# Kernel tuning notes

Hardware: AMD Instinct MI355X
Metric: run time of the kernel (lower is better)

The kernel has to match this reference:

```python
import jax, jax.numpy as jnp
import numpy as np


def _dwconv(x, w, pad):
    # depthwise conv, x: [B,C,H,W], w: [C,1,kh,kw]
    return jax.lax.conv_general_dilated(
        x, w, (1, 1), [(pad, pad), (pad, pad)],
        dimension_numbers=('NCHW', 'OIHW', 'NCHW'),
        feature_group_count=x.shape[1])


def _hw_to_wh(x, h, w):
    # rearrange 'b (h w) c -> b (w h) c'
    b, t, c = x.shape
    return x.reshape(b, h, w, c).transpose(0, 2, 1, 3).reshape(b, t, c)


def _wkv(decay, first, k, v):
    # Vision-RWKV WKV: decay/first [C4]; k, v [B, T, C4]
    w_neg = -jnp.exp(decay)  # RUN_CUDA applies w = -exp(w)
    u = first

    def step(carry, kv):
        p, q, o = carry
        kt, vt = kv
        no = jnp.maximum(o, u + kt)
        A = jnp.exp(o - no)
        Bx = jnp.exp(u + kt - no)
        y = (A * p + Bx * vt) / (A * q + Bx)
        no2 = jnp.maximum(o + w_neg, kt)
        A2 = jnp.exp(o + w_neg - no2)
        B2 = jnp.exp(kt - no2)
        return (A2 * p + B2 * vt, A2 * q + B2, no2), y

    Bn, T, C4 = k.shape
    init = (jnp.zeros((Bn, C4), k.dtype), jnp.zeros((Bn, C4), k.dtype),
            jnp.full((Bn, C4), -1e38, k.dtype))
    _, ys = jax.lax.scan(step, init, (jnp.swapaxes(k, 0, 1), jnp.swapaxes(v, 0, 1)))
    return jnp.swapaxes(ys, 0, 1)  # [B, T, C4]


def setup_inputs() -> dict:
    key = jax.random.key(0)
    ks = jax.random.split(key, 16)
    B, H, W, C = 8, 64, 64, 256
    T = H * W
    C4 = 4 * C
    s = 1.0 / np.sqrt(C)
    return {
        'x': jax.random.normal(ks[0], (B, T, C), jnp.float32),
        'alpha': jax.random.normal(ks[1], (4,), jnp.float32) * 0.5,
        'dw1': jax.random.normal(ks[2], (C, 1, 1, 1), jnp.float32) * s,
        'dw3': jax.random.normal(ks[3], (C, 1, 3, 3), jnp.float32) * s,
        'dw5': jax.random.normal(ks[4], (C, 1, 5, 5), jnp.float32) * s,
        'Wk': jax.random.normal(ks[5], (C, C), jnp.float32) * s,
        'Wv': jax.random.normal(ks[6], (C, C), jnp.float32) * s,
        'Wr': jax.random.normal(ks[7], (C, C), jnp.float32) * s,
        'Wf': jax.random.normal(ks[8], (C, C), jnp.float32) * s,
        'bf': jax.random.normal(ks[9], (C,), jnp.float32) * 0.02,
        'Wb': jax.random.normal(ks[10], (C, C), jnp.float32) * s,
        'bb': jax.random.normal(ks[11], (C,), jnp.float32) * 0.02,
        'spatial_decay': jax.random.normal(ks[12], (C4,), jnp.float32),
        'spatial_first': jax.random.normal(ks[13], (C4,), jnp.float32),
        'Wo': jax.random.normal(ks[14], (C, C4), jnp.float32) * (1.0 / np.sqrt(C4)),
        'h': H,
        'w': W,
    }


def reference(x, alpha, dw1, dw3, dw5, Wk, Wv, Wr, Wf, bf, Wb, bb,
              spatial_decay, spatial_first, Wo, h, w):
    B, T, C = x.shape
    # OmniShift (training path): alpha-weighted identity + depthwise 1/3/5 convs
    xi = x.reshape(B, h, w, C).transpose(0, 3, 1, 2)  # [B,C,H,W]
    xsft = (alpha[0] * xi + alpha[1] * _dwconv(xi, dw1, 0)
            + alpha[2] * _dwconv(xi, dw3, 1) + alpha[3] * _dwconv(xi, dw5, 2))
    xf = xsft.transpose(0, 2, 3, 1).reshape(B, T, C)  # [B,T,C]
    k = xf @ Wk.T
    v = xf @ Wv.T
    sr = jax.nn.sigmoid(xf @ Wr.T)
    # 1x1 conv1d over channels == linear with bias
    k1 = k @ Wf.T + bf
    v1 = v @ Wf.T + bf
    k3 = k @ Wb.T + bb
    v3 = v @ Wb.T + bb
    k2 = _hw_to_wh(k1, h, w)
    v2 = _hw_to_wh(v1, h, w)
    k4 = _hw_to_wh(k3, h, w)
    v4 = _hw_to_wh(v3, h, w)
    ks_ = jnp.concatenate([k1, k2, k3, k4], axis=2)  # [B,T,4C]
    vs_ = jnp.concatenate([v1, v2, v3, v4], axis=2)
    srs = jnp.concatenate([sr, sr, sr, sr], axis=2)
    Tf = jnp.asarray(T, x.dtype)
    xs = _wkv(spatial_decay / Tf, spatial_first / Tf, ks_, vs_)
    return (xs * srs) @ Wo.T  # [B,T,C]
```

## Files before the change

kernel.cpp:

```cpp
#include <hip/hip_runtime.h>

typedef __attribute__((ext_vector_type(8))) short bf16x8;
typedef __attribute__((ext_vector_type(4))) float f32x4;
typedef __attribute__((ext_vector_type(4))) unsigned short u16x4;
typedef __attribute__((ext_vector_type(2))) unsigned short u16x2;
typedef __attribute__((ext_vector_type(8))) unsigned short u16x8;

#define GLD16(g, l) __builtin_amdgcn_global_load_lds( \
    (const __attribute__((address_space(1))) void*)(g), \
    (__attribute__((address_space(3))) void*)(l), 16, 0, 0)

__device__ __forceinline__ unsigned short f2bf(float f) {
  unsigned u = __float_as_uint(f);
  unsigned r = u + 0x7FFFu + ((u >> 16) & 1u);
  return (unsigned short)(r >> 16);
}
__device__ __forceinline__ float bf2f(unsigned short h) {
  return __uint_as_float(((unsigned)h) << 16);
}

template <int N>
__device__ __forceinline__ void wait_vm() {
  if constexpr (N == 0) asm volatile("s_waitcnt vmcnt(0)" ::: "memory");
  else if constexpr (N == 6) asm volatile("s_waitcnt vmcnt(6)" ::: "memory");
  else if constexpr (N == 8) asm volatile("s_waitcnt vmcnt(8)" ::: "memory");
  else static_assert(N == 0, "unsupported vmcnt");
}


__global__ void k_weff(const float* __restrict__ alpha,
                       const float* __restrict__ dw1,
                       const float* __restrict__ dw3,
                       const float* __restrict__ dw5,
                       float* __restrict__ weff) {
  int tap = blockIdx.x;
  int c = threadIdx.x;
  int dy = tap / 5, dx = tap % 5;
  float v = alpha[3] * dw5[c * 25 + tap];
  if (dy >= 1 && dy <= 3 && dx >= 1 && dx <= 3)
    v += alpha[2] * dw3[c * 9 + (dy - 1) * 3 + (dx - 1)];
  if (tap == 12) v += alpha[1] * dw1[c] + alpha[0];
  weff[tap * 256 + c] = v;
}

__global__ void k_combine(const float* __restrict__ Wk,
                          const float* __restrict__ Wv,
                          const float* __restrict__ Wr,
                          const float* __restrict__ Wf,
                          const float* __restrict__ Wb,
                          const float* __restrict__ bfv,
                          const float* __restrict__ bbv,
                          short* __restrict__ wcat,
                          float* __restrict__ bias) {
  int mat = blockIdx.x >> 8;
  int i = blockIdx.x & 255;
  int j = threadIdx.x;
  if (mat == 4) {
    wcat[(size_t)(1024 + i) * 256 + j] = (short)f2bf(Wr[i * 256 + j]);
    if (j == 0) bias[1024 + i] = 0.f;
    return;
  }
  const float* Am = (mat & 1) ? Wb : Wf;
  const float* Bm = (mat < 2) ? Wk : Wv;
  const float* arow = Am + i * 256;
  float acc = 0.f;
  for (int m = 0; m < 256; ++m) acc += arow[m] * Bm[m * 256 + j];
  int newrow = ((mat & 1) << 9) + (i << 1) + (mat >> 1);
  wcat[(size_t)newrow * 256 + j] = (short)f2bf(acc);
  if (j == 0) bias[newrow] = (mat & 1) ? bbv[i] : bfv[i];
}

__global__ void k_wo(const float* __restrict__ Wo, short* __restrict__ wob) {
  int i = blockIdx.x * 256 + threadIdx.x;
  wob[i] = (short)f2bf(Wo[i]);
}

__global__ __launch_bounds__(256, 8)
void k_shift(const float* __restrict__ x, const float* __restrict__ weff,
             unsigned short* __restrict__ xf) {
  int c = threadIdx.x;
  int w0 = blockIdx.x * 8;
  int h0 = blockIdx.y * 2;
  int b = blockIdx.z;

  float wg[5][5];
#pragma unroll
  for (int dy = 0; dy < 5; ++dy)
#pragma unroll
    for (int dx = 0; dx < 5; ++dx)
      wg[dy][dx] = weff[(dy * 5 + dx) * 256 + c];

  const float* xb = x + (size_t)b * 4096 * 256 + c;
  int rowoff[6];
  bool rv[6];
#pragma unroll
  for (int r = 0; r < 6; ++r) {
    int y = h0 + r - 2;
    rv[r] = (y >= 0 && y < 64);
    int yc = y < 0 ? 0 : (y > 63 ? 63 : y);
    rowoff[r] = yc * 64 * 256;
  }

  float win[6][8];
#pragma unroll
  for (int j = -2; j <= 1; ++j) {
    int xx = w0 + j;
    int slot = j & 7;
    bool xv = (xx >= 0);
    int xc = xx < 0 ? 0 : xx;
#pragma unroll
    for (int r = 0; r < 6; ++r) {
      float v = xb[rowoff[r] + xc * 256];
      win[r][slot] = (xv && rv[r]) ? v : 0.f;
    }
  }

  unsigned short* xo = xf + ((size_t)b * 4096 + (size_t)h0 * 64) * 256 + c;
#pragma unroll
  for (int ui = 0; ui < 8; ++ui) {
    int w = w0 + ui;
    {
      int xx = w + 2;
      int slot = (ui + 2) & 7;
      bool xv = (xx < 64);
      int xc = xx > 63 ? 63 : xx;
#pragma unroll
      for (int r = 0; r < 6; ++r) {
        float v = xb[rowoff[r] + xc * 256];
        win[r][slot] = (xv && rv[r]) ? v : 0.f;
      }
    }
#pragma unroll
    for (int j = 0; j < 2; ++j) {
      float a0 = 0.f, a1 = 0.f, a2 = 0.f, a3 = 0.f, a4 = 0.f;
#pragma unroll
      for (int dx = 0; dx < 5; ++dx) {
        int slot = (ui - 2 + dx) & 7;
        a0 = fmaf(win[j + 0][slot], wg[0][dx], a0);
        a1 = fmaf(win[j + 1][slot], wg[1][dx], a1);
        a2 = fmaf(win[j + 2][slot], wg[2][dx], a2);
        a3 = fmaf(win[j + 3][slot], wg[3][dx], a3);
        a4 = fmaf(win[j + 4][slot], wg[4][dx], a4);
      }
      xo[((size_t)j * 64 + w) * 256] = f2bf(((a0 + a1) + (a2 + a3)) + a4);
    }
  }
}

template <int EPI, int BM, int BK, int SWZ>
__global__ __launch_bounds__(256, (BM == 128) ? 2 : 3)
void gemm_db(const short* __restrict__ A, const short* __restrict__ Bm,
             const float* __restrict__ bias,
             void* __restrict__ O0, void* __restrict__ O1,
             int M, int N, int K) {
  constexpr int AE = BM * BK;
  constexpr int BUFS = (BM + 128) * BK;
  constexpr int MI = BM / 32;
  constexpr int CH = BK / 8;
  constexpr int LA = BM * BK / 2048;
  constexpr int LB = BK / 16;
  constexpr int LD = LA + LB;
  constexpr int RW = 132;
  __shared__ __align__(16) short lds[2 * BUFS];

  int t = threadIdx.x;
  int lane = t & 63, wv = t >> 6;
  int wr = wv >> 1, wc = wv & 1;
  int m0, n0;
  if (SWZ) {
    int x = blockIdx.x & 7;
    int j = blockIdx.x >> 3;
    m0 = (x * 32 + j / 10) * BM;
    n0 = (j % 10) * 128;
  } else {
    m0 = blockIdx.x * BM;
    n0 = blockIdx.y * 128;
  }
  const int NK = K / BK;
  f32x4 acc[MI][4] = {};

  float bb[4];
  if (EPI == 0) {
#pragma unroll
    for (int ni = 0; ni < 4; ++ni)
      bb[ni] = bias[n0 + wc * 64 + ni * 16 + (lane & 15)];
  }

  auto STAGE = [&](int step, int bo) {
    int k0 = step * BK;
#pragma unroll
    for (int i = 0; i < LA; ++i) {
      int cc = t + i * 256;
      int row = cc / CH, kc = cc % CH;
      GLD16(A + (size_t)(m0 + row) * K + k0 + ((kc ^ (row & (CH - 1))) << 3),
            &lds[bo + cc * 8]);
    }
#pragma unroll
    for (int i = 0; i < LB; ++i) {
      int cc = t + i * 256;
      int row = cc / CH, kc = cc % CH;
      GLD16(Bm + (size_t)(n0 + row) * K + k0 + ((kc ^ (row & (CH - 1))) << 3),
            &lds[bo + AE + cc * 8]);
    }
  };
  auto COMPUTE = [&](int bo) {
#pragma unroll
    for (int kk = 0; kk < BK / 32; ++kk) {
      int ch = kk * 4 + (lane >> 4);
      bf16x8 av[MI], bv[4];
#pragma unroll
      for (int i = 0; i < MI; ++i) {
        int row = wr * (BM / 2) + i * 16 + (lane & 15);
        av[i] = *(const bf16x8*)&lds[bo + row * BK + ((ch ^ (row & (CH - 1))) << 3)];
      }
#pragma unroll
      for (int i = 0; i < 4; ++i) {
        int row = wc * 64 + i * 16 + (lane & 15);
        bv[i] = *(const bf16x8*)&lds[bo + AE + row * BK + ((ch ^ (row & (CH - 1))) << 3)];
      }
#pragma unroll
      for (int mi = 0; mi < MI; ++mi)
#pragma unroll
        for (int ni = 0; ni < 4; ++ni)
          acc[mi][ni] = __builtin_amdgcn_mfma_f32_16x16x32_bf16(av[mi], bv[ni], acc[mi][ni], 0, 0, 0);
    }
  };

  STAGE(0, 0);
  STAGE(1, BUFS);
#pragma unroll
  for (int k = 0; k < 16; ++k) {
    if (k >= NK) break;
    int bo = (k & 1) ? BUFS : 0;
    if (k < NK - 1) wait_vm<LD>();
    else wait_vm<0>();
    __builtin_amdgcn_s_barrier();
    COMPUTE(bo);
    asm volatile("s_waitcnt lgkmcnt(0)" ::: "memory");
    __builtin_amdgcn_s_barrier();
    if (k + 2 < NK) STAGE(k + 2, bo);
  }

  float* fl = (float*)lds;
  int rrow = t >> 3;
  int colb = (t & 7) * 16;
#pragma unroll
  for (int mi = 0; mi < MI; ++mi) {
    if (mi) __syncthreads();
    {
      int r0 = (lane >> 4) * 4;
#pragma unroll
      for (int ni = 0; ni < 4; ++ni) {
        int colL = wc * 64 + (lane & 15) + ni * 16;
        f32x4 v = acc[mi][ni];
#pragma unroll
        for (int j = 0; j < 4; ++j) {
          float vj = v[j];
          if (EPI == 0) vj += bb[ni];
          fl[(wr * 16 + r0 + j) * RW + colL] = vj;
        }
      }
    }
    __syncthreads();
    float vv[16];
#pragma unroll
    for (int q = 0; q < 4; ++q)
      *(f32x4*)&vv[q * 4] = *(const f32x4*)&fl[rrow * RW + colb + q * 4];
    int grow = m0 + (rrow >> 4) * (BM / 2) + mi * 16 + (rrow & 15);
    if (EPI == 0) {
      u16x8 o0, o1;
      if (n0 < 1024) {
#pragma unroll
        for (int q = 0; q < 8; ++q) { o0[q] = f2bf(vv[q]); o1[q] = f2bf(vv[8 + q]); }
        unsigned short* dst = (unsigned short*)O0 + (size_t)grow * 1024 + n0 + colb;
        *(u16x8*)dst = o0;
        *(u16x8*)(dst + 8) = o1;
      } else {
#pragma unroll
        for (int q = 0; q < 8; ++q) {
          o0[q] = f2bf(1.f / (1.f + __expf(-vv[q])));
          o1[q] = f2bf(1.f / (1.f + __expf(-vv[8 + q])));
        }
        unsigned short* dst = (unsigned short*)O1 + (size_t)grow * 256 + (n0 - 1024) + colb;
        *(u16x8*)dst = o0;
        *(u16x8*)(dst + 8) = o1;
      }
    } else {
      float* dst = (float*)O0 + (size_t)grow * N + n0 + colb;
#pragma unroll
      for (int q = 0; q < 4; ++q) {
        f32x4 ov = {vv[q * 4], vv[q * 4 + 1], vv[q * 4 + 2], vv[q * 4 + 3]};
        *(f32x4*)(dst + q * 4) = ov;
      }
    }
  }
}

__global__ __launch_bounds__(256, 8)
void k_wkv(const unsigned short* __restrict__ kvb, const unsigned short* __restrict__ srb,
           const float* __restrict__ decay, const float* __restrict__ first,
           unsigned short* __restrict__ xssr) {
  const int T = 4096;
  int tid = threadIdx.x;
  int g = tid >> 7;
  int l = tid & 127;
  int c0 = l * 2;
  int tr = blockIdx.y;
  int s = (g << 1) | tr;
  int scol = s * 256;
  int chunk = blockIdx.x;
  int b = blockIdx.z;
  const float invT = 1.0f / 4096.0f;

  float P0 = 0.f, P1 = 0.f, Q0 = 0.f, Q1 = 0.f;
  float D0 = __expf(-__expf(decay[scol + c0] * invT));
  float D1 = __expf(-__expf(decay[scol + c0 + 1] * invT));
  float eu0 = __expf(first[scol + c0] * invT);
  float eu1 = __expf(first[scol + c0 + 1] * invT);

  int t0 = chunk * 32;
  int tstart = t0 >= 16 ? t0 - 16 : 0;
  int tend = t0 + 32;
  const size_t bT = (size_t)b * T;
  const int kvoff = (g << 9) + (c0 << 1);

  auto kvload = [&](int tt) {
    int tok = tr ? (((tt & 63) << 6) | (tt >> 6)) : tt;
    return *(const u16x4*)(kvb + (bT + tok) * 1024 + kvoff);
  };
  auto srload = [&](int tt) {
    return *(const u16x2*)(srb + (bT + tt) * 256 + c0);
  };

  u16x4 kvA = kvload(tstart);
  u16x4 kvB = kvload(tstart + 1);
  u16x2 svA = srload(tstart);
  u16x2 svB = srload(tstart + 1);

  for (int tt = tstart; tt < tend; tt += 2) {
    int tp2 = tt + 2 < tend ? tt + 2 : tend - 1;
    int tp3 = tt + 3 < tend ? tt + 3 : tend - 1;
    u16x4 kvC = kvload(tp2);
    u16x4 kvD = kvload(tp3);
    u16x2 svC = srload(tp2);
    u16x2 svD = srload(tp3);

#pragma unroll
    for (int u = 0; u < 2; ++u) {
      int ti = tt + u;
      u16x4 kv4 = u ? kvB : kvA;
      u16x2 sv = u ? svB : svA;
      float k0 = bf2f(kv4[0]), v0 = bf2f(kv4[1]);
      float k1 = bf2f(kv4[2]), v1 = bf2f(kv4[3]);
      float e0 = __expf(k0), e1 = __expf(k1);
      if (ti >= t0) {
        float t0e = e0 * eu0, t1e = e1 * eu1;
        float y0 = fmaf(t0e, v0, P0) * __builtin_amdgcn_rcpf(Q0 + t0e);
        float y1 = fmaf(t1e, v1, P1) * __builtin_amdgcn_rcpf(Q1 + t1e);
        u16x2 ow;
        ow[0] = f2bf(y0 * bf2f(sv[0]));
        ow[1] = f2bf(y1 * bf2f(sv[1]));
        *(u16x2*)(xssr + (bT + ti) * 1024 + scol + c0) = ow;
      }
      P0 = fmaf(P0, D0, e0 * v0);
      Q0 = fmaf(Q0, D0, e0);
      P1 = fmaf(P1, D1, e1 * v1);
      Q1 = fmaf(Q1, D1, e1);
    }
    kvA = kvC; kvB = kvD;
    svA = svC; svB = svD;
  }
}

extern "C" void kernel_launch(void* const* d_in, const int* in_sizes, int n_in,
                              void* d_out, int out_size, void* d_ws, size_t ws_size,
                              hipStream_t stream) {
  const float* x      = (const float*)d_in[0];
  const float* alpha  = (const float*)d_in[1];
  const float* dw1    = (const float*)d_in[2];
  const float* dw3    = (const float*)d_in[3];
  const float* dw5    = (const float*)d_in[4];
  const float* Wk     = (const float*)d_in[5];
  const float* Wv     = (const float*)d_in[6];
  const float* Wr     = (const float*)d_in[7];
  const float* Wf     = (const float*)d_in[8];
  const float* bfv    = (const float*)d_in[9];
  const float* Wb     = (const float*)d_in[10];
  const float* bbv    = (const float*)d_in[11];
  const float* sdecay = (const float*)d_in[12];
  const float* sfirst = (const float*)d_in[13];
  const float* Wo     = (const float*)d_in[14];
  (void)n_in; (void)out_size; (void)ws_size;

  const int Bn = in_sizes[0] / (4096 * 256);
  const int MT = Bn * 4096;

  char* ws = (char*)d_ws;
  size_t off = 0;
  auto alloc = [&](size_t bytes) {
    void* p = ws + off;
    off += (bytes + 255) & ~(size_t)255;
    return p;
  };
  short* xf            = (short*)alloc((size_t)MT * 256 * 2);
  unsigned short* kv   = (unsigned short*)alloc((size_t)MT * 1024 * 2);
  unsigned short* srb  = (unsigned short*)alloc((size_t)MT * 256 * 2);
  unsigned short* xssr = (unsigned short*)alloc((size_t)MT * 1024 * 2);
  short* wcat          = (short*)alloc((size_t)1280 * 256 * 2);
  float* bias          = (float*)alloc(1280 * 4);
  float* weff          = (float*)alloc(25 * 256 * 4);
  short* wob           = (short*)alloc((size_t)256 * 1024 * 2);

  k_weff<<<25, 256, 0, stream>>>(alpha, dw1, dw3, dw5, weff);
  k_combine<<<1280, 256, 0, stream>>>(Wk, Wv, Wr, Wf, Wb, bfv, bbv, wcat, bias);
  k_wo<<<1024, 256, 0, stream>>>(Wo, wob);
  k_shift<<<dim3(8, 32, Bn), 256, 0, stream>>>(x, weff, (unsigned short*)xf);
  gemm_db<0, 128, 64, 1><<<dim3(MT / 128 * 10), 256, 0, stream>>>(
      xf, wcat, bias, kv, srb, MT, 1280, 256);
  k_wkv<<<dim3(128, 2, Bn), 256, 0, stream>>>(kv, srb, sdecay, sfirst, xssr);
  gemm_db<1, 64, 64, 0><<<dim3(MT / 64, 2), 256, 0, stream>>>(
      (const short*)xssr, wob, nullptr, d_out, nullptr, MT, 256, 1024);
}
```

Measured before the change: 165.9 us.

## Add single-buffered high-occupancy GEMM for projection and swizzle output GEMM grid

```diff
diff --git a/kernel.cpp b/kernel.cpp
--- a/kernel.cpp
+++ b/kernel.cpp
@@ -147,8 +147,136 @@
   }
 }
 
-template <int EPI, int BM, int BK, int SWZ>
-__global__ __launch_bounds__(256, (BM == 128) ? 2 : 3)
+template <int EPI, int BM, int BK, int NT>
+__global__ __launch_bounds__(256, 5)
+void gemm_bt(const short* __restrict__ A, const short* __restrict__ Bm,
+             const float* __restrict__ bias,
+             void* __restrict__ O0, void* __restrict__ O1,
+             int M, int N, int K) {
+  constexpr int AE = BM * BK;
+  constexpr int MI = BM / 32;
+  constexpr int CH = BK / 8;
+  constexpr int LA = BM * BK / 2048;
+  constexpr int LB = BK / 16;
+  constexpr int RW = 132;
+  __shared__ __align__(16) short lds[AE + 128 * BK];
+
+  int t = threadIdx.x;
+  int lane = t & 63, wv = t >> 6;
+  int wr = wv >> 1, wc = wv & 1;
+  int m0, n0;
+  if (NT) {
+    int x = blockIdx.x & 7;
+    int j = blockIdx.x >> 3;
+    int mpx = M / (BM * 8);
+    m0 = (x * mpx + j / NT) * BM;
+    n0 = (j % NT) * 128;
+  } else {
+    m0 = blockIdx.x * BM;
+    n0 = blockIdx.y * 128;
+  }
+  f32x4 acc[MI][4] = {};
+
+  for (int k0 = 0; k0 < K; k0 += BK) {
+#pragma unroll
+    for (int i = 0; i < LA; ++i) {
+      int cc = t + i * 256;
+      int row = cc / CH, kc = cc % CH;
+      GLD16(A + (size_t)(m0 + row) * K + k0 + ((kc ^ (row & (CH - 1))) << 3), &lds[cc * 8]);
+    }
+#pragma unroll
+    for (int i = 0; i < LB; ++i) {
+      int cc = t + i * 256;
+      int row = cc / CH, kc = cc % CH;
+      GLD16(Bm + (size_t)(n0 + row) * K + k0 + ((kc ^ (row & (CH - 1))) << 3), &lds[AE + cc * 8]);
+    }
+    __syncthreads();
+#pragma unroll
+    for (int kk = 0; kk < BK / 32; ++kk) {
+      int ch = kk * 4 + (lane >> 4);
+      bf16x8 av[MI], bv[4];
+#pragma unroll
+      for (int i = 0; i < MI; ++i) {
+        int row = wr * (BM / 2) + i * 16 + (lane & 15);
+        av[i] = *(const bf16x8*)&lds[row * BK + ((ch ^ (row & (CH - 1))) << 3)];
+      }
+#pragma unroll
+      for (int i = 0; i < 4; ++i) {
+        int row = wc * 64 + i * 16 + (lane & 15);
+        bv[i] = *(const bf16x8*)&lds[AE + row * BK + ((ch ^ (row & (CH - 1))) << 3)];
+      }
+#pragma unroll
+      for (int mi = 0; mi < MI; ++mi)
+#pragma unroll
+        for (int ni = 0; ni < 4; ++ni)
+          acc[mi][ni] = __builtin_amdgcn_mfma_f32_16x16x32_bf16(av[mi], bv[ni], acc[mi][ni], 0, 0, 0);
+    }
+    __syncthreads();
+  }
+
+  float* fl = (float*)lds;
+  float bb[4];
+  if (EPI == 0) {
+#pragma unroll
+    for (int ni = 0; ni < 4; ++ni)
+      bb[ni] = bias[n0 + wc * 64 + ni * 16 + (lane & 15)];
+  }
+  int rrow = t >> 3;
+  int colb = (t & 7) * 16;
+#pragma unroll
+  for (int mi = 0; mi < MI; ++mi) {
+    if (mi) __syncthreads();
+    {
+      int r0 = (lane >> 4) * 4;
+#pragma unroll
+      for (int ni = 0; ni < 4; ++ni) {
+        int colL = wc * 64 + (lane & 15) + ni * 16;
+        f32x4 v = acc[mi][ni];
+#pragma unroll
+        for (int j = 0; j < 4; ++j) {
+          float vj = v[j];
+          if (EPI == 0) vj += bb[ni];
+          fl[(wr * 16 + r0 + j) * RW + colL] = vj;
+        }
+      }
+    }
+    __syncthreads();
+    float vv[16];
+#pragma unroll
+    for (int q = 0; q < 4; ++q)
+      *(f32x4*)&vv[q * 4] = *(const f32x4*)&fl[rrow * RW + colb + q * 4];
+    int grow = m0 + (rrow >> 4) * (BM / 2) + mi * 16 + (rrow & 15);
+    if (EPI == 0) {
+      u16x8 o0, o1;
+      if (n0 < 1024) {
+#pragma unroll
+        for (int q = 0; q < 8; ++q) { o0[q] = f2bf(vv[q]); o1[q] = f2bf(vv[8 + q]); }
+        unsigned short* dst = (unsigned short*)O0 + (size_t)grow * 1024 + n0 + colb;
+        *(u16x8*)dst = o0;
+        *(u16x8*)(dst + 8) = o1;
+      } else {
+#pragma unroll
+        for (int q = 0; q < 8; ++q) {
+          o0[q] = f2bf(1.f / (1.f + __expf(-vv[q])));
+          o1[q] = f2bf(1.f / (1.f + __expf(-vv[8 + q])));
+        }
+        unsigned short* dst = (unsigned short*)O1 + (size_t)grow * 256 + (n0 - 1024) + colb;
+        *(u16x8*)dst = o0;
+        *(u16x8*)(dst + 8) = o1;
+      }
+    } else {
+      float* dst = (float*)O0 + (size_t)grow * N + n0 + colb;
+#pragma unroll
+      for (int q = 0; q < 4; ++q) {
+        f32x4 ov = {vv[q * 4], vv[q * 4 + 1], vv[q * 4 + 2], vv[q * 4 + 3]};
+        *(f32x4*)(dst + q * 4) = ov;
+      }
+    }
+  }
+}
+
+template <int EPI, int BM, int BK, int NT>
+__global__ __launch_bounds__(256, 3)
 void gemm_db(const short* __restrict__ A, const short* __restrict__ Bm,
              const float* __restrict__ bias,
              void* __restrict__ O0, void* __restrict__ O1,
@@ -167,11 +295,12 @@
   int lane = t & 63, wv = t >> 6;
   int wr = wv >> 1, wc = wv & 1;
   int m0, n0;
-  if (SWZ) {
+  if (NT) {
     int x = blockIdx.x & 7;
     int j = blockIdx.x >> 3;
-    m0 = (x * 32 + j / 10) * BM;
-    n0 = (j % 10) * 128;
+    int mpx = M / (BM * 8);
+    m0 = (x * mpx + j / NT) * BM;
+    n0 = (j % NT) * 128;
   } else {
     m0 = blockIdx.x * BM;
     n0 = blockIdx.y * 128;
@@ -415,9 +544,9 @@
   k_combine<<<1280, 256, 0, stream>>>(Wk, Wv, Wr, Wf, Wb, bfv, bbv, wcat, bias);
   k_wo<<<1024, 256, 0, stream>>>(Wo, wob);
   k_shift<<<dim3(8, 32, Bn), 256, 0, stream>>>(x, weff, (unsigned short*)xf);
-  gemm_db<0, 128, 64, 1><<<dim3(MT / 128 * 10), 256, 0, stream>>>(
+  gemm_bt<0, 128, 64, 10><<<dim3(MT / 128 * 10), 256, 0, stream>>>(
       xf, wcat, bias, kv, srb, MT, 1280, 256);
   k_wkv<<<dim3(128, 2, Bn), 256, 0, stream>>>(kv, srb, sdecay, sfirst, xssr);
-  gemm_db<1, 64, 64, 0><<<dim3(MT / 64, 2), 256, 0, stream>>>(
+  gemm_db<1, 64, 64, 2><<<dim3(MT / 64 * 2), 256, 0, stream>>>(
       (const short*)xssr, wob, nullptr, d_out, nullptr, MT, 256, 1024);
 }
```

New measurement: 188.0 us. 13.3% more time.
